# Performance work log

Hardware: AMD Instinct MI355X
Metric: run time of the kernel (lower is better)

The kernel has to match this reference:

```python
import jax, jax.numpy as jnp
import numpy as np
import math

D_MODEL = 512
N_HEADS = 8
FACTOR = 5
B, L_Q, L_K = 8, 4096, 4096


def setup_inputs() -> dict:
    key = jax.random.key(0)
    ks = jax.random.split(key, 9)
    s = 0.02
    sample_k = max(1, int(FACTOR * math.log(L_K + 1)))  # 41
    return {
        "query": jax.random.normal(ks[0], (B, L_Q, D_MODEL), jnp.float32),
        "key_in": jax.random.normal(ks[1], (B, L_K, D_MODEL), jnp.float32),
        "value": jax.random.normal(ks[2], (B, L_K, D_MODEL), jnp.float32),
        "W_Q": jax.random.normal(ks[3], (D_MODEL, D_MODEL), jnp.float32) * s,
        "W_K": jax.random.normal(ks[4], (D_MODEL, D_MODEL), jnp.float32) * s,
        "W_V": jax.random.normal(ks[5], (D_MODEL, D_MODEL), jnp.float32) * s,
        "W_out": jax.random.normal(ks[6], (D_MODEL, D_MODEL), jnp.float32) * s,
        "b_out": jnp.zeros((D_MODEL,), jnp.float32),
        "sample_idx": jax.random.randint(ks[8], (L_Q, sample_k), 0, L_K),
    }


def reference(query, key_in, value, W_Q, W_K, W_V, W_out, b_out, sample_idx):
    b, lq, _ = query.shape
    lk = key_in.shape[1]
    H = N_HEADS
    E = D_MODEL // H
    # projections -> [B, H, L, E]
    Q = (query @ W_Q).reshape(b, lq, H, E).transpose(0, 2, 1, 3)
    K = (key_in @ W_K).reshape(b, lk, H, E).transpose(0, 2, 1, 3)
    V = (value @ W_V).reshape(b, lk, H, E).transpose(0, 2, 1, 3)

    u = max(1, int(FACTOR * math.log(lq + 1)))  # top-u queries (41)

    # sparsity proxy M(q_i, K) on randomly sampled keys
    K_sample = K[:, :, sample_idx, :]                      # [B,H,L_Q,S,E]
    QK_sample = jnp.einsum('bhqe,bhqse->bhqs', Q, K_sample)
    M = QK_sample.max(axis=-1) - QK_sample.mean(axis=-1)   # [B,H,L_Q]
    _, M_top = jax.lax.top_k(M, u)                         # [B,H,u]

    # attention for the top-u queries only
    Q_reduce = jnp.take_along_axis(Q, M_top[..., None], axis=2)  # [B,H,u,E]
    scale = 1.0 / math.sqrt(E)
    scores = jnp.einsum('bhue,bhke->bhuk', Q_reduce, K) * scale
    attn = jax.nn.softmax(scores, axis=-1)  # dropout is identity (eval)
    ctx_top = jnp.einsum('bhuk,bhke->bhue', attn, V)       # [B,H,u,E]

    # mean-value context for the lazy queries, scatter-update the active ones
    ctx = jnp.broadcast_to(V.mean(axis=2, keepdims=True), (b, H, lq, E))
    bi = jnp.arange(b)[:, None, None]
    hi = jnp.arange(H)[None, :, None]
    ctx = ctx.at[bi, hi, M_top].set(ctx_top)

    ctx = ctx.transpose(0, 2, 1, 3).reshape(b, lq, H * E)
    return ctx @ W_out + b_out
```

## Files before the change

kernel.cpp:

```cpp
#include <hip/hip_runtime.h>
#include <cstdint>
#include <cstddef>

#define D_MODEL 512
#define NHEADS  8
#define EDIM    64
#define BATCH   8
#define LSEQ    4096

typedef unsigned short u16;
typedef __attribute__((ext_vector_type(8))) short short8;
typedef __attribute__((ext_vector_type(4))) float f32x4;

__device__ __forceinline__ u16 bf16_rne(float x) {
  unsigned int u = __float_as_uint(x);
  u += 0x7FFFu + ((u >> 16) & 1u);
  return (u16)(u >> 16);
}
__device__ __forceinline__ void split2(float x, u16& h, u16& l) {
  h = bf16_rne(x);
  float hf = __uint_as_float((unsigned int)h << 16);
  l = bf16_rne(x - hf);
}

__global__ __launch_bounds__(256) void cvt_w(
    const float* __restrict__ W0, const float* __restrict__ W1,
    const float* __restrict__ W2, const float* __restrict__ W3,
    u16* __restrict__ out) {
  const float* W = (blockIdx.z == 0) ? W0 : ((blockIdx.z == 1) ? W1 :
                   ((blockIdx.z == 2) ? W2 : W3));
  u16* P = out + (size_t)blockIdx.z * 524288;
  __shared__ float tile[64][65];
  const int k0 = blockIdx.x * 64, n0 = blockIdx.y * 64;
  const int t = threadIdx.x;
  const int tr = t >> 4, tc = (t & 15) * 4;
#pragma unroll
  for (int j = 0; j < 4; ++j) {
    int kr = tr + j * 16;
    float4 v = *(const float4*)(W + (size_t)(k0 + kr) * 512 + n0 + tc);
    tile[kr][tc + 0] = v.x; tile[kr][tc + 1] = v.y;
    tile[kr][tc + 2] = v.z; tile[kr][tc + 3] = v.w;
  }
  __syncthreads();
#pragma unroll
  for (int j = 0; j < 4; ++j) {
    int nr = tr + j * 16;
    ushort4 h, l;
    split2(tile[tc + 0][nr], h.x, l.x);
    split2(tile[tc + 1][nr], h.y, l.y);
    split2(tile[tc + 2][nr], h.z, l.z);
    split2(tile[tc + 3][nr], h.w, l.w);
    size_t off = (size_t)(n0 + nr) * 512 + k0 + tc;
    *(ushort4*)(P + off) = h;
    *(ushort4*)(P + 262144 + off) = l;
  }
}

__device__ __forceinline__ void gld_lds16(const char* g, char* l) {
  __builtin_amdgcn_global_load_lds((const __attribute__((address_space(1))) void*)g,
                                   (__attribute__((address_space(3))) void*)l, 16, 0, 0);
}

__global__ __launch_bounds__(256, 2) void gemm_fused(
    const float* __restrict__ X0, const float* __restrict__ X1,
    const float* __restrict__ X2, const u16* __restrict__ WPbase,
    float* __restrict__ Y0, float* __restrict__ Y1, float* __restrict__ Y2) {
  __shared__ u16 Ah[2][128 * 40];
  __shared__ u16 Al[2][128 * 40];
  __shared__ u16 Bh[2][128 * 32];
  __shared__ u16 Bl[2][128 * 32];
  const int z = blockIdx.z;
  const float* X = (z == 0) ? X0 : ((z == 1) ? X1 : X2);
  float* Y = (z == 0) ? Y0 : ((z == 1) ? Y1 : Y2);
  const u16* WP = WPbase + (size_t)z * 524288;

  const int tid = threadIdx.x;
  const int lane = tid & 63, wv = tid >> 6;
  const int wm = (wv & 1) * 64, wn = (wv >> 1) * 64;
  const int bn = blockIdx.x * 128, bm = blockIdx.y * 128;
  const int fr = lane & 15, quad = lane >> 4;
  const int sRow = tid >> 2, sColB = (tid & 3) * 16;
  const int ar = tid >> 1, ac = (tid & 1) * 16;

  f32x4 acc[16];
#pragma unroll
  for (int i = 0; i < 16; ++i) acc[i] = (f32x4){0.f, 0.f, 0.f, 0.f};

  const u16* Wh = WP;
  const u16* Wl = WP + 262144;
  const float* Arow = X + (size_t)(bm + ar) * 512 + ac;

  union V8 { ushort4 v4[2]; short8 v8; };

  {
    float4 x0 = *(const float4*)(Arow);
    float4 x1 = *(const float4*)(Arow + 4);
    float4 x2 = *(const float4*)(Arow + 8);
    float4 x3 = *(const float4*)(Arow + 12);
#pragma unroll
    for (int j = 0; j < 2; ++j) {
      const size_t rB = (size_t)(bn + j * 64 + sRow) * 512;
      const int lo = (j * 256 + wv * 64) * 16;
      gld_lds16((const char*)(Wh + rB) + sColB, (char*)Bh[0] + lo);
      gld_lds16((const char*)(Wl + rB) + sColB, (char*)Bl[0] + lo);
    }
    V8 h0, l0, h1, l1;
    split2(x0.x, h0.v4[0].x, l0.v4[0].x);
    split2(x0.y, h0.v4[0].y, l0.v4[0].y);
    split2(x0.z, h0.v4[0].z, l0.v4[0].z);
    split2(x0.w, h0.v4[0].w, l0.v4[0].w);
    split2(x1.x, h0.v4[1].x, l0.v4[1].x);
    split2(x1.y, h0.v4[1].y, l0.v4[1].y);
    split2(x1.z, h0.v4[1].z, l0.v4[1].z);
    split2(x1.w, h0.v4[1].w, l0.v4[1].w);
    split2(x2.x, h1.v4[0].x, l1.v4[0].x);
    split2(x2.y, h1.v4[0].y, l1.v4[0].y);
    split2(x2.z, h1.v4[0].z, l1.v4[0].z);
    split2(x2.w, h1.v4[0].w, l1.v4[0].w);
    split2(x3.x, h1.v4[1].x, l1.v4[1].x);
    split2(x3.y, h1.v4[1].y, l1.v4[1].y);
    split2(x3.z, h1.v4[1].z, l1.v4[1].z);
    split2(x3.w, h1.v4[1].w, l1.v4[1].w);
    *(short8*)&Ah[0][ar * 40 + ac]     = h0.v8;
    *(short8*)&Ah[0][ar * 40 + ac + 8] = h1.v8;
    *(short8*)&Al[0][ar * 40 + ac]     = l0.v8;
    *(short8*)&Al[0][ar * 40 + ac + 8] = l1.v8;
  }
  __syncthreads();

  for (int kk = 0; kk < 16; ++kk) {
    const int cur = kk & 1, nxt = cur ^ 1;
    float4 x0, x1, x2, x3;
    if (kk < 15) {
      x0 = *(const float4*)(Arow + (kk + 1) * 32);
      x1 = *(const float4*)(Arow + (kk + 1) * 32 + 4);
      x2 = *(const float4*)(Arow + (kk + 1) * 32 + 8);
      x3 = *(const float4*)(Arow + (kk + 1) * 32 + 12);
#pragma unroll
      for (int j = 0; j < 2; ++j) {
        const size_t rB = (size_t)(bn + j * 64 + sRow) * 512 + (kk + 1) * 32;
        const int lo = (j * 256 + wv * 64) * 16;
        gld_lds16((const char*)(Wh + rB) + sColB, (char*)Bh[nxt] + lo);
        gld_lds16((const char*)(Wl + rB) + sColB, (char*)Bl[nxt] + lo);
      }
    }
    short8 ah[4], al[4], bh4[4], bl4[4];
#pragma unroll
    for (int mi = 0; mi < 4; ++mi) {
      ah[mi] = *(const short8*)&Ah[cur][(wm + mi * 16 + fr) * 40 + quad * 8];
      al[mi] = *(const short8*)&Al[cur][(wm + mi * 16 + fr) * 40 + quad * 8];
    }
#pragma unroll
    for (int ni = 0; ni < 4; ++ni) {
      bh4[ni] = *(const short8*)&Bh[cur][(wn + ni * 16 + fr) * 32 + quad * 8];
      bl4[ni] = *(const short8*)&Bl[cur][(wn + ni * 16 + fr) * 32 + quad * 8];
    }
#pragma unroll
    for (int mi = 0; mi < 4; ++mi)
#pragma unroll
      for (int ni = 0; ni < 4; ++ni)
        acc[mi * 4 + ni] = __builtin_amdgcn_mfma_f32_16x16x32_bf16(
            ah[mi], bh4[ni], acc[mi * 4 + ni], 0, 0, 0);
#pragma unroll
    for (int mi = 0; mi < 4; ++mi)
#pragma unroll
      for (int ni = 0; ni < 4; ++ni)
        acc[mi * 4 + ni] = __builtin_amdgcn_mfma_f32_16x16x32_bf16(
            ah[mi], bl4[ni], acc[mi * 4 + ni], 0, 0, 0);
#pragma unroll
    for (int mi = 0; mi < 4; ++mi)
#pragma unroll
      for (int ni = 0; ni < 4; ++ni)
        acc[mi * 4 + ni] = __builtin_amdgcn_mfma_f32_16x16x32_bf16(
            al[mi], bh4[ni], acc[mi * 4 + ni], 0, 0, 0);
    if (kk < 15) {
      V8 h0, l0, h1, l1;
      split2(x0.x, h0.v4[0].x, l0.v4[0].x);
      split2(x0.y, h0.v4[0].y, l0.v4[0].y);
      split2(x0.z, h0.v4[0].z, l0.v4[0].z);
      split2(x0.w, h0.v4[0].w, l0.v4[0].w);
      split2(x1.x, h0.v4[1].x, l0.v4[1].x);
      split2(x1.y, h0.v4[1].y, l0.v4[1].y);
      split2(x1.z, h0.v4[1].z, l0.v4[1].z);
      split2(x1.w, h0.v4[1].w, l0.v4[1].w);
      split2(x2.x, h1.v4[0].x, l1.v4[0].x);
      split2(x2.y, h1.v4[0].y, l1.v4[0].y);
      split2(x2.z, h1.v4[0].z, l1.v4[0].z);
      split2(x2.w, h1.v4[0].w, l1.v4[0].w);
      split2(x3.x, h1.v4[1].x, l1.v4[1].x);
      split2(x3.y, h1.v4[1].y, l1.v4[1].y);
      split2(x3.z, h1.v4[1].z, l1.v4[1].z);
      split2(x3.w, h1.v4[1].w, l1.v4[1].w);
      *(short8*)&Ah[nxt][ar * 40 + ac]     = h0.v8;
      *(short8*)&Ah[nxt][ar * 40 + ac + 8] = h1.v8;
      *(short8*)&Al[nxt][ar * 40 + ac]     = l0.v8;
      *(short8*)&Al[nxt][ar * 40 + ac + 8] = l1.v8;
    }
    __syncthreads();
  }
#pragma unroll
  for (int mi = 0; mi < 4; ++mi)
#pragma unroll
    for (int ni = 0; ni < 4; ++ni) {
      const f32x4 a = acc[mi * 4 + ni];
      float* yp = Y + (size_t)(bm + wm + mi * 16 + quad * 4) * 512 + (bn + wn + ni * 16 + fr);
#pragma unroll
      for (int r = 0; r < 4; ++r) yp[(size_t)r * 512] = a[r];
    }
}

__global__ __launch_bounds__(256) void qk_sample_half(
    const float* __restrict__ Q, const float* __restrict__ K,
    const int* __restrict__ sidx, float* __restrict__ M, int S, int hg) {
  const int blk = blockIdx.x;
  const int lane = threadIdx.x & 63;
  const int b = blk & 7;
  const int q = ((blk >> 3) << 2) + (threadIdx.x >> 6);
  const int s = lane >> 5;
  const int hl = (lane >> 3) & 3;
  const int d = lane & 7;
  const int h = hg * 4 + hl;
  const int col = hg * 256 + hl * 64 + d * 8;

  const float* Qp = Q + ((size_t)b * LSEQ + q) * D_MODEL + col;
  const float4 q0 = *(const float4*)Qp;
  const float4 q1 = *(const float4*)(Qp + 4);
  const float* Kb = K + (size_t)b * LSEQ * D_MODEL + col;
  const int* sp = sidx + (size_t)q * S;

  auto rowp = [&](int j) -> const float* {
    int jj = j + s;
    int row = sp[(jj < S) ? jj : (S - 1)];
    return Kb + (size_t)row * D_MODEL;
  };

  const float* pr0 = rowp(0);
  float4 a0 = *(const float4*)pr0, b0 = *(const float4*)(pr0 + 4);
  const float* pr1 = rowp(2);
  float4 a1 = *(const float4*)pr1, b1 = *(const float4*)(pr1 + 4);

  float mx = -3.4e38f, sum = 0.0f;
  for (int j = 0; j < S; j += 2) {
    const float4 ca = a0, cb = b0;
    a0 = a1; b0 = b1;
    const float* pn = rowp(j + 4);
    a1 = *(const float4*)pn;
    b1 = *(const float4*)(pn + 4);
    float p = ca.x * q0.x + ca.y * q0.y + ca.z * q0.z + ca.w * q0.w +
              cb.x * q1.x + cb.y * q1.y + cb.z * q1.z + cb.w * q1.w;
    p += __shfl_xor(p, 1, 64);
    p += __shfl_xor(p, 2, 64);
    p += __shfl_xor(p, 4, 64);
    if (j + s < S) {
      mx = fmaxf(mx, p);
      sum += p;
    }
  }
  mx = fmaxf(mx, __shfl_xor(mx, 32, 64));
  sum += __shfl_xor(sum, 32, 64);
  if (s == 0 && d == 0)
    M[((size_t)(b * NHEADS + h)) * LSEQ + q] = mx - sum / (float)S;
}

__global__ __launch_bounds__(256) void topk_kernel(
    const float* __restrict__ M, int* __restrict__ Mtop, int U) {
  __shared__ float vals[LSEQ];
  __shared__ float wbest[4];
  __shared__ int widx[4];
  int bh = blockIdx.x;
  int t = threadIdx.x;
  const int w = t >> 6, lane = t & 63;
  for (int i = t; i < LSEQ; i += 256) vals[i] = M[(size_t)bh * LSEQ + i];
  __syncthreads();
  for (int it = 0; it < U; ++it) {
    float best = -3.4e38f; int bi = 0x7fffffff;
    for (int i = t; i < LSEQ; i += 256) {
      float v = vals[i];
      if (v > best) { best = v; bi = i; }
    }
#pragma unroll
    for (int o = 1; o < 64; o <<= 1) {
      float ov = __shfl_xor(best, o, 64);
      int oi = __shfl_xor(bi, o, 64);
      if (ov > best || (ov == best && oi < bi)) { best = ov; bi = oi; }
    }
    if (lane == 0) { wbest[w] = best; widx[w] = bi; }
    __syncthreads();
    if (t == 0) {
      float B = wbest[0]; int I = widx[0];
#pragma unroll
      for (int w2 = 1; w2 < 4; ++w2)
        if (wbest[w2] > B || (wbest[w2] == B && widx[w2] < I)) {
          B = wbest[w2]; I = widx[w2];
        }
      Mtop[(size_t)bh * U + it] = I;
      vals[I] = -3.4e38f;
    }
    __syncthreads();
  }
}

__global__ __launch_bounds__(256, 2) void attn_flash(
    const float* __restrict__ Q, const float* __restrict__ K,
    const float* __restrict__ V, const int* __restrict__ Mtop,
    float* __restrict__ part_ctx, float* __restrict__ part_m,
    float* __restrict__ part_l, int U, int nsplit, int chunks_per_block) {
  __shared__ u16 KhS[64 * 72];
  __shared__ u16 KlS[64 * 72];
  __shared__ float VsS[64 * 68];
  const int bh = blockIdx.y, split = blockIdx.x;
  const int h = bh & (NHEADS - 1), b = bh >> 3;
  const int t = threadIdx.x, w = t >> 6, lane = t & 63;
  const int fr = lane & 15, quad = lane >> 4;

  const int qi = w * 16 + fr;
  const int qrow = (qi < U) ? Mtop[(size_t)bh * U + qi] : Mtop[(size_t)bh * U];
  const float4* Qr = (const float4*)(Q + ((size_t)(b * LSEQ) + qrow) * D_MODEL + h * EDIM);
  float4 qa = Qr[quad * 2], qb = Qr[quad * 2 + 1];
  float4 qc = Qr[quad * 2 + 8], qd = Qr[quad * 2 + 9];
  short8 qh0, ql0, qh1, ql1;
  {
    u16 hh, ll;
    split2(qa.x, hh, ll); qh0[0] = (short)hh; ql0[0] = (short)ll;
    split2(qa.y, hh, ll); qh0[1] = (short)hh; ql0[1] = (short)ll;
    split2(qa.z, hh, ll); qh0[2] = (short)hh; ql0[2] = (short)ll;
    split2(qa.w, hh, ll); qh0[3] = (short)hh; ql0[3] = (short)ll;
    split2(qb.x, hh, ll); qh0[4] = (short)hh; ql0[4] = (short)ll;
    split2(qb.y, hh, ll); qh0[5] = (short)hh; ql0[5] = (short)ll;
    split2(qb.z, hh, ll); qh0[6] = (short)hh; ql0[6] = (short)ll;
    split2(qb.w, hh, ll); qh0[7] = (short)hh; ql0[7] = (short)ll;
    split2(qc.x, hh, ll); qh1[0] = (short)hh; ql1[0] = (short)ll;
    split2(qc.y, hh, ll); qh1[1] = (short)hh; ql1[1] = (short)ll;
    split2(qc.z, hh, ll); qh1[2] = (short)hh; ql1[2] = (short)ll;
    split2(qc.w, hh, ll); qh1[3] = (short)hh; ql1[3] = (short)ll;
    split2(qd.x, hh, ll); qh1[4] = (short)hh; ql1[4] = (short)ll;
    split2(qd.y, hh, ll); qh1[5] = (short)hh; ql1[5] = (short)ll;
    split2(qd.z, hh, ll); qh1[6] = (short)hh; ql1[6] = (short)ll;
    split2(qd.w, hh, ll); qh1[7] = (short)hh; ql1[7] = (short)ll;
  }

  float4 c4[16];
#pragma unroll
  for (int i = 0; i < 16; ++i) c4[i] = make_float4(0.f, 0.f, 0.f, 0.f);
  float m = -1e30f, l = 0.0f;

  const int r = t >> 2, cg = t & 3;

  const int k_base = split * (chunks_per_block * 64);
  for (int c = 0; c < chunks_per_block; ++c) {
    const int k0 = k_base + c * 64;
    const float4* Kg4 = (const float4*)(K + ((size_t)(b * LSEQ) + k0 + r) * D_MODEL + h * EDIM);
    const float4* Vg4 = (const float4*)(V + ((size_t)(b * LSEQ) + k0 + r) * D_MODEL + h * EDIM);
#pragma unroll
    for (int i = 0; i < 4; ++i) {
      const int f4 = cg + 4 * i;
      float4 kv = Kg4[f4];
      float4 vv = Vg4[f4];
      ushort4 hh, ll;
      split2(kv.x, hh.x, ll.x);
      split2(kv.y, hh.y, ll.y);
      split2(kv.z, hh.z, ll.z);
      split2(kv.w, hh.w, ll.w);
      *(ushort4*)&KhS[r * 72 + f4 * 4] = hh;
      *(ushort4*)&KlS[r * 72 + f4 * 4] = ll;
      *(float4*)&VsS[r * 68 + f4 * 4] = vv;
    }
    __syncthreads();

    f32x4 acc[4];
#pragma unroll
    for (int mt = 0; mt < 4; ++mt) acc[mt] = (f32x4){0.f, 0.f, 0.f, 0.f};
#pragma unroll
    for (int mt = 0; mt < 4; ++mt) {
      short8 kh = *(const short8*)&KhS[(mt * 16 + fr) * 72 + quad * 8];
      short8 kl = *(const short8*)&KlS[(mt * 16 + fr) * 72 + quad * 8];
      acc[mt] = __builtin_amdgcn_mfma_f32_16x16x32_bf16(kh, qh0, acc[mt], 0, 0, 0);
      acc[mt] = __builtin_amdgcn_mfma_f32_16x16x32_bf16(kh, ql0, acc[mt], 0, 0, 0);
      acc[mt] = __builtin_amdgcn_mfma_f32_16x16x32_bf16(kl, qh0, acc[mt], 0, 0, 0);
    }
#pragma unroll
    for (int mt = 0; mt < 4; ++mt) {
      short8 kh = *(const short8*)&KhS[(mt * 16 + fr) * 72 + 32 + quad * 8];
      short8 kl = *(const short8*)&KlS[(mt * 16 + fr) * 72 + 32 + quad * 8];
      acc[mt] = __builtin_amdgcn_mfma_f32_16x16x32_bf16(kh, qh1, acc[mt], 0, 0, 0);
      acc[mt] = __builtin_amdgcn_mfma_f32_16x16x32_bf16(kh, ql1, acc[mt], 0, 0, 0);
      acc[mt] = __builtin_amdgcn_mfma_f32_16x16x32_bf16(kl, qh1, acc[mt], 0, 0, 0);
    }

    float cm = -3.4e38f;
#pragma unroll
    for (int mt = 0; mt < 4; ++mt) {
#pragma unroll
      for (int rr = 0; rr < 4; ++rr) {
        float s = acc[mt][rr] * 0.125f;
        acc[mt][rr] = s;
        cm = fmaxf(cm, s);
      }
    }
    cm = fmaxf(cm, __shfl_xor(cm, 16, 64));
    cm = fmaxf(cm, __shfl_xor(cm, 32, 64));
    float mn = fmaxf(m, cm);
    if (mn > m) {
      float f = __expf(m - mn);
      l *= f;
#pragma unroll
      for (int i = 0; i < 16; ++i) {
        c4[i].x *= f; c4[i].y *= f; c4[i].z *= f; c4[i].w *= f;
      }
      m = mn;
    }
    float psum = 0.0f;
#pragma unroll
    for (int mt = 0; mt < 4; ++mt) {
#pragma unroll
      for (int rr = 0; rr < 4; ++rr) {
        float p = __expf(acc[mt][rr] - m);
        acc[mt][rr] = p;
        psum += p;
      }
    }
    l += psum;

#pragma unroll
    for (int mt = 0; mt < 4; ++mt) {
#pragma unroll
      for (int rr = 0; rr < 4; ++rr) {
        const int krow = mt * 16 + quad * 4 + rr;
        const float4* vr = (const float4*)&VsS[krow * 68];
        const float p = acc[mt][rr];
#pragma unroll
        for (int i = 0; i < 16; ++i) {
          float4 vv = vr[i];
          c4[i].x += p * vv.x; c4[i].y += p * vv.y;
          c4[i].z += p * vv.z; c4[i].w += p * vv.w;
        }
      }
    }
    __syncthreads();
  }

#pragma unroll
  for (int i = 0; i < 16; ++i) {
    c4[i].x += __shfl_xor(c4[i].x, 16, 64);
    c4[i].y += __shfl_xor(c4[i].y, 16, 64);
    c4[i].z += __shfl_xor(c4[i].z, 16, 64);
    c4[i].w += __shfl_xor(c4[i].w, 16, 64);
    c4[i].x += __shfl_xor(c4[i].x, 32, 64);
    c4[i].y += __shfl_xor(c4[i].y, 32, 64);
    c4[i].z += __shfl_xor(c4[i].z, 32, 64);
    c4[i].w += __shfl_xor(c4[i].w, 32, 64);
  }
  l += __shfl_xor(l, 16, 64);
  l += __shfl_xor(l, 32, 64);

  if (quad == 0 && qi < U) {
    part_m[(size_t)(bh * nsplit + split) * 64 + qi] = m;
    part_l[(size_t)(bh * nsplit + split) * 64 + qi] = l;
  }
  float* pc = part_ctx + (size_t)(bh * nsplit + split) * 4096;
  if (quad == 0) {
#pragma unroll
    for (int ii = 0; ii < 16; ++ii) pc[ii * 64 + qi] = (&c4[ii >> 2].x)[ii & 3];
  } else if (quad == 1) {
#pragma unroll
    for (int ii = 0; ii < 16; ++ii) pc[(16 + ii) * 64 + qi] = (&c4[4 + (ii >> 2)].x)[ii & 3];
  } else if (quad == 2) {
#pragma unroll
    for (int ii = 0; ii < 16; ++ii) pc[(32 + ii) * 64 + qi] = (&c4[8 + (ii >> 2)].x)[ii & 3];
  } else {
#pragma unroll
    for (int ii = 0; ii < 16; ++ii) pc[(48 + ii) * 64 + qi] = (&c4[12 + (ii >> 2)].x)[ii & 3];
  }
}

__global__ __launch_bounds__(256) void attn_combine(
    const float* __restrict__ part_ctx, const float* __restrict__ part_m,
    const float* __restrict__ part_l, float* __restrict__ ctxTop,
    int U, int nsplit) {
  __shared__ float F[16][64];
  const int bh = blockIdx.x;
  const int t = threadIdx.x, lane = t & 63, grp = t >> 6;
  if (grp == 0) {
    float M = -3.4e38f;
    for (int s = 0; s < nsplit; ++s)
      M = fmaxf(M, part_m[(size_t)(bh * nsplit + s) * 64 + lane]);
    float L = 0.0f;
    for (int s = 0; s < nsplit; ++s)
      L += part_l[(size_t)(bh * nsplit + s) * 64 + lane] *
           __expf(part_m[(size_t)(bh * nsplit + s) * 64 + lane] - M);
    float invL = 1.0f / L;
    for (int s = 0; s < nsplit; ++s)
      F[s][lane] = __expf(part_m[(size_t)(bh * nsplit + s) * 64 + lane] - M) * invL;
  }
  __syncthreads();
  for (int ei = 0; ei < 16; ++ei) {
    int e = grp * 16 + ei;
    float acc = 0.0f;
    for (int s = 0; s < nsplit; ++s)
      acc += F[s][lane] * part_ctx[(size_t)(bh * nsplit + s) * 4096 + e * 64 + lane];
    if (lane < U) ctxTop[((size_t)bh * U + lane) * 64 + e] = acc;
  }
}

__global__ __launch_bounds__(256) void vmean_part(
    const float* __restrict__ V, float* __restrict__ Vm) {
  __shared__ float part[4][EDIM];
  const int bh = blockIdx.x, chunk = blockIdx.y;
  const int h = bh & (NHEADS - 1), b = bh >> 3;
  const int t = threadIdx.x;
  const int e = t & 63, c = t >> 6;
  float s = 0.0f;
  const int k0 = chunk * 512 + c * 128;
  for (int k = k0; k < k0 + 128; ++k)
    s += V[((size_t)b * LSEQ + k) * D_MODEL + h * EDIM + e];
  part[c][e] = s;
  __syncthreads();
  if (c == 0)
    atomicAdd(&Vm[(size_t)bh * EDIM + e],
              (part[0][e] + part[1][e] + part[2][e] + part[3][e]) *
                  (1.0f / (float)LSEQ));
}

__global__ __launch_bounds__(256) void base_out_kernel(
    const float* __restrict__ Vm, const float* __restrict__ Wout,
    const float* __restrict__ bout, float* __restrict__ base) {
  __shared__ float cb[D_MODEL];
  int b = blockIdx.x;
  int t = threadIdx.x;
  for (int d = t; d < D_MODEL; d += 256) cb[d] = Vm[(size_t)b * D_MODEL + d];
  __syncthreads();
  for (int n = t; n < D_MODEL; n += 256) {
    float s = bout[n];
    for (int d = 0; d < D_MODEL; ++d) s += cb[d] * Wout[(size_t)d * D_MODEL + n];
    base[(size_t)b * D_MODEL + n] = s;
  }
}

__global__ __launch_bounds__(256) void fill_out(
    const float* __restrict__ base, float* __restrict__ out) {
  size_t i = (size_t)blockIdx.x * 256 + threadIdx.x;
  int n4 = (int)(i & 127);
  size_t bq = i >> 7;
  int b = (int)(bq >> 12);
  float4 v = ((const float4*)base)[(size_t)b * 128 + n4];
  ((float4*)out)[i] = v;
}

__global__ __launch_bounds__(256, 1) void delta_out_mfma(
    const float* __restrict__ ctxTop, const float* __restrict__ Vm,
    const int* __restrict__ Mtop, const u16* __restrict__ WoutTP,
    float* __restrict__ out, int U) {
  __shared__ u16 Dh[64 * 72];
  __shared__ u16 Dl[64 * 72];
  __shared__ int qr[64];
  const int bh = blockIdx.x;
  const int h = bh & (NHEADS - 1), b = bh >> 3;
  const int t = threadIdx.x, lane = t & 63, wv = t >> 6;
  const int fr = lane & 15, quad = lane >> 4;

  {
    const int r = t >> 2, c0 = (t & 3) * 16;
#pragma unroll
    for (int j = 0; j < 4; ++j) {
      float4 v = make_float4(0.f, 0.f, 0.f, 0.f);
      if (r < U) {
        float4 cv = *(const float4*)(ctxTop + ((size_t)bh * U + r) * EDIM + c0 + j * 4);
        float4 mv = *(const float4*)(Vm + (size_t)bh * EDIM + c0 + j * 4);
        v = make_float4(cv.x - mv.x, cv.y - mv.y, cv.z - mv.z, cv.w - mv.w);
      }
      ushort4 hh, ll;
      split2(v.x, hh.x, ll.x);
      split2(v.y, hh.y, ll.y);
      split2(v.z, hh.z, ll.z);
      split2(v.w, hh.w, ll.w);
      *(ushort4*)&Dh[r * 72 + c0 + j * 4] = hh;
      *(ushort4*)&Dl[r * 72 + c0 + j * 4] = ll;
    }
  }
  if (t < 64) qr[t] = (t < U) ? Mtop[(size_t)bh * U + t] : -1;
  __syncthreads();

  f32x4 acc[32];
#pragma unroll
  for (int i = 0; i < 32; ++i) acc[i] = (f32x4){0.f, 0.f, 0.f, 0.f};

  const u16* Wh = WoutTP;
  const u16* Wl = WoutTP + 262144;

#pragma unroll
  for (int ks = 0; ks < 2; ++ks) {
    short8 a_h[4], a_l[4];
#pragma unroll
    for (int mt = 0; mt < 4; ++mt) {
      a_h[mt] = *(const short8*)&Dh[(mt * 16 + fr) * 72 + ks * 32 + quad * 8];
      a_l[mt] = *(const short8*)&Dl[(mt * 16 + fr) * 72 + ks * 32 + quad * 8];
    }
#pragma unroll
    for (int nt = 0; nt < 8; ++nt) {
      const int n = wv * 128 + nt * 16 + fr;
      const size_t off = (size_t)n * 512 + h * EDIM + ks * 32 + quad * 8;
      short8 b_h = *(const short8*)&Wh[off];
      short8 b_l = *(const short8*)&Wl[off];
#pragma unroll
      for (int mt = 0; mt < 4; ++mt) {
        acc[mt * 8 + nt] = __builtin_amdgcn_mfma_f32_16x16x32_bf16(
            a_h[mt], b_h, acc[mt * 8 + nt], 0, 0, 0);
        acc[mt * 8 + nt] = __builtin_amdgcn_mfma_f32_16x16x32_bf16(
            a_h[mt], b_l, acc[mt * 8 + nt], 0, 0, 0);
        acc[mt * 8 + nt] = __builtin_amdgcn_mfma_f32_16x16x32_bf16(
            a_l[mt], b_h, acc[mt * 8 + nt], 0, 0, 0);
      }
    }
  }

  int qreg[16];
#pragma unroll
  for (int mt = 0; mt < 4; ++mt)
#pragma unroll
    for (int r4 = 0; r4 < 4; ++r4) qreg[mt * 4 + r4] = qr[mt * 16 + quad * 4 + r4];
#pragma unroll
  for (int mt = 0; mt < 4; ++mt)
#pragma unroll
    for (int nt = 0; nt < 8; ++nt) {
      const f32x4 a = acc[mt * 8 + nt];
      const int n = wv * 128 + nt * 16 + fr;
#pragma unroll
      for (int r4 = 0; r4 < 4; ++r4) {
        const int q = qreg[mt * 4 + r4];
        if (q >= 0)
          atomicAdd(out + ((size_t)b * LSEQ + q) * D_MODEL + n, a[r4]);
      }
    }
}

extern "C" void kernel_launch(void* const* d_in, const int* in_sizes, int n_in,
                              void* d_out, int out_size, void* d_ws, size_t ws_size,
                              hipStream_t stream) {
  const float* query  = (const float*)d_in[0];
  const float* key_in = (const float*)d_in[1];
  const float* value  = (const float*)d_in[2];
  const float* W_Q    = (const float*)d_in[3];
  const float* W_K    = (const float*)d_in[4];
  const float* W_V    = (const float*)d_in[5];
  const float* W_out  = (const float*)d_in[6];
  const float* b_out  = (const float*)d_in[7];
  const int*   sidx   = (const int*)d_in[8];
  float* out = (float*)d_out;

  const int S = in_sizes[8] / LSEQ;
  const int U = S;

  char* ws = (char*)d_ws;
  size_t o = 0;
  float* Qf     = (float*)(ws + o); o += (size_t)BATCH * LSEQ * D_MODEL * 4;
  float* Kf     = (float*)(ws + o); o += (size_t)BATCH * LSEQ * D_MODEL * 4;
  float* Vf     = (float*)(ws + o); o += (size_t)BATCH * LSEQ * D_MODEL * 4;
  int*   Mtop   = (int*)  (ws + o); o += ((size_t)64 * U * 4 + 255) & ~255ULL;
  float* ctxTop = (float*)(ws + o); o += ((size_t)64 * U * EDIM * 4 + 255) & ~255ULL;
  float* Vm     = (float*)(ws + o); o += 16384;
  float* baseO  = (float*)(ws + o); o += 16384;
  u16*   Wpl    = (u16*)  (ws + o); o += (size_t)4 * 524288 * 2;
  size_t unionOff = o;

  float* M = (float*)(ws + unionOff);
  int nsplit = 16;
  for (;;) {
    size_t need = unionOff + 2 * ((size_t)64 * nsplit * 64 * 4)
                  + (size_t)64 * nsplit * 4096 * 4;
    if (need <= ws_size || nsplit == 1) break;
    nsplit >>= 1;
  }
  float* part_m   = (float*)(ws + unionOff);
  float* part_l   = part_m + (size_t)64 * nsplit * 64;
  float* part_ctx = part_l + (size_t)64 * nsplit * 64;
  const int chunks_per_block = 64 / nsplit;

  cvt_w<<<dim3(8, 8, 4), 256, 0, stream>>>(W_Q, W_K, W_V, W_out, Wpl);
  gemm_fused<<<dim3(4, 256, 3), 256, 0, stream>>>(
      query, key_in, value, Wpl, Qf, Kf, Vf);

  qk_sample_half<<<(BATCH * LSEQ) / 4, 256, 0, stream>>>(Qf, Kf, sidx, M, S, 0);
  qk_sample_half<<<(BATCH * LSEQ) / 4, 256, 0, stream>>>(Qf, Kf, sidx, M, S, 1);
  topk_kernel<<<BATCH * NHEADS, 256, 0, stream>>>(M, Mtop, U);
  attn_flash<<<dim3(nsplit, BATCH * NHEADS), 256, 0, stream>>>(
      Qf, Kf, Vf, Mtop, part_ctx, part_m, part_l, U, nsplit, chunks_per_block);
  attn_combine<<<BATCH * NHEADS, 256, 0, stream>>>(
      part_ctx, part_m, part_l, ctxTop, U, nsplit);
  hipMemsetAsync(Vm, 0, (size_t)BATCH * NHEADS * EDIM * 4, stream);
  vmean_part<<<dim3(BATCH * NHEADS, 8), 256, 0, stream>>>(Vf, Vm);
  base_out_kernel<<<BATCH, 256, 0, stream>>>(Vm, W_out, b_out, baseO);
  fill_out<<<(BATCH * LSEQ * (D_MODEL / 4)) / 256, 256, 0, stream>>>(baseO, out);
  delta_out_mfma<<<BATCH * NHEADS, 256, 0, stream>>>(
      ctxTop, Vm, Mtop, Wpl + (size_t)3 * 524288, out, U);
}
```

Baseline: 827.9 us.

## Swizzle packed weight layout for conflict-free LDS reads, drop GEMM double buffering

The weight pre-pack kernel now XOR-swizzles the 8-element k-chunks within each 32-wide group by row, and both the projection GEMM and the output-projection consumer read with the matching swizzled offset. The B tile in LDS (rows of 32 u16) then avoids bank conflicts on the MFMA operand reads. The GEMM also drops its double-buffered LDS pipeline in favour of a single buffer with load, sync, compute, sync per k-step. That halves shared memory and may raise occupancy, but global-load latency is no longer overlapped with MFMA work.

```diff
diff --git a/kernel.cpp b/kernel.cpp
--- a/kernel.cpp
+++ b/kernel.cpp
@@ -50,7 +50,8 @@
     split2(tile[tc + 1][nr], h.y, l.y);
     split2(tile[tc + 2][nr], h.z, l.z);
     split2(tile[tc + 3][nr], h.w, l.w);
-    size_t off = (size_t)(n0 + nr) * 512 + k0 + tc;
+    const int tcs = (tc & 36) | (((((tc >> 3) & 3)) ^ (nr & 3)) << 3);
+    size_t off = (size_t)(n0 + nr) * 512 + k0 + tcs;
     *(ushort4*)(P + off) = h;
     *(ushort4*)(P + 262144 + off) = l;
   }
@@ -65,10 +66,10 @@
     const float* __restrict__ X0, const float* __restrict__ X1,
     const float* __restrict__ X2, const u16* __restrict__ WPbase,
     float* __restrict__ Y0, float* __restrict__ Y1, float* __restrict__ Y2) {
-  __shared__ u16 Ah[2][128 * 40];
-  __shared__ u16 Al[2][128 * 40];
-  __shared__ u16 Bh[2][128 * 32];
-  __shared__ u16 Bl[2][128 * 32];
+  __shared__ u16 Ah[128 * 40];
+  __shared__ u16 Al[128 * 40];
+  __shared__ u16 Bh[128 * 32];
+  __shared__ u16 Bl[128 * 32];
   const int z = blockIdx.z;
   const float* X = (z == 0) ? X0 : ((z == 1) ? X1 : X2);
   float* Y = (z == 0) ? Y0 : ((z == 1) ? Y1 : Y2);
@@ -79,6 +80,7 @@
   const int wm = (wv & 1) * 64, wn = (wv >> 1) * 64;
   const int bn = blockIdx.x * 128, bm = blockIdx.y * 128;
   const int fr = lane & 15, quad = lane >> 4;
+  const int bq = (quad ^ (fr & 3)) * 8;
   const int sRow = tid >> 2, sColB = (tid & 3) * 16;
   const int ar = tid >> 1, ac = (tid & 1) * 16;
 
@@ -92,17 +94,17 @@
 
   union V8 { ushort4 v4[2]; short8 v8; };
 
-  {
-    float4 x0 = *(const float4*)(Arow);
-    float4 x1 = *(const float4*)(Arow + 4);
-    float4 x2 = *(const float4*)(Arow + 8);
-    float4 x3 = *(const float4*)(Arow + 12);
+  for (int kk = 0; kk < 16; ++kk) {
+    float4 x0 = *(const float4*)(Arow + kk * 32);
+    float4 x1 = *(const float4*)(Arow + kk * 32 + 4);
+    float4 x2 = *(const float4*)(Arow + kk * 32 + 8);
+    float4 x3 = *(const float4*)(Arow + kk * 32 + 12);
 #pragma unroll
     for (int j = 0; j < 2; ++j) {
-      const size_t rB = (size_t)(bn + j * 64 + sRow) * 512;
+      const size_t rB = (size_t)(bn + j * 64 + sRow) * 512 + kk * 32;
       const int lo = (j * 256 + wv * 64) * 16;
-      gld_lds16((const char*)(Wh + rB) + sColB, (char*)Bh[0] + lo);
-      gld_lds16((const char*)(Wl + rB) + sColB, (char*)Bl[0] + lo);
+      gld_lds16((const char*)(Wh + rB) + sColB, (char*)Bh + lo);
+      gld_lds16((const char*)(Wl + rB) + sColB, (char*)Bl + lo);
     }
     V8 h0, l0, h1, l1;
     split2(x0.x, h0.v4[0].x, l0.v4[0].x);
@@ -121,39 +123,21 @@
     split2(x3.y, h1.v4[1].y, l1.v4[1].y);
     split2(x3.z, h1.v4[1].z, l1.v4[1].z);
     split2(x3.w, h1.v4[1].w, l1.v4[1].w);
-    *(short8*)&Ah[0][ar * 40 + ac]     = h0.v8;
-    *(short8*)&Ah[0][ar * 40 + ac + 8] = h1.v8;
-    *(short8*)&Al[0][ar * 40 + ac]     = l0.v8;
-    *(short8*)&Al[0][ar * 40 + ac + 8] = l1.v8;
-  }
-  __syncthreads();
-
-  for (int kk = 0; kk < 16; ++kk) {
-    const int cur = kk & 1, nxt = cur ^ 1;
-    float4 x0, x1, x2, x3;
-    if (kk < 15) {
-      x0 = *(const float4*)(Arow + (kk + 1) * 32);
-      x1 = *(const float4*)(Arow + (kk + 1) * 32 + 4);
-      x2 = *(const float4*)(Arow + (kk + 1) * 32 + 8);
-      x3 = *(const float4*)(Arow + (kk + 1) * 32 + 12);
-#pragma unroll
-      for (int j = 0; j < 2; ++j) {
-        const size_t rB = (size_t)(bn + j * 64 + sRow) * 512 + (kk + 1) * 32;
-        const int lo = (j * 256 + wv * 64) * 16;
-        gld_lds16((const char*)(Wh + rB) + sColB, (char*)Bh[nxt] + lo);
-        gld_lds16((const char*)(Wl + rB) + sColB, (char*)Bl[nxt] + lo);
-      }
-    }
+    *(short8*)&Ah[ar * 40 + ac]     = h0.v8;
+    *(short8*)&Ah[ar * 40 + ac + 8] = h1.v8;
+    *(short8*)&Al[ar * 40 + ac]     = l0.v8;
+    *(short8*)&Al[ar * 40 + ac + 8] = l1.v8;
+    __syncthreads();
     short8 ah[4], al[4], bh4[4], bl4[4];
 #pragma unroll
     for (int mi = 0; mi < 4; ++mi) {
-      ah[mi] = *(const short8*)&Ah[cur][(wm + mi * 16 + fr) * 40 + quad * 8];
-      al[mi] = *(const short8*)&Al[cur][(wm + mi * 16 + fr) * 40 + quad * 8];
+      ah[mi] = *(const short8*)&Ah[(wm + mi * 16 + fr) * 40 + quad * 8];
+      al[mi] = *(const short8*)&Al[(wm + mi * 16 + fr) * 40 + quad * 8];
     }
 #pragma unroll
     for (int ni = 0; ni < 4; ++ni) {
-      bh4[ni] = *(const short8*)&Bh[cur][(wn + ni * 16 + fr) * 32 + quad * 8];
-      bl4[ni] = *(const short8*)&Bl[cur][(wn + ni * 16 + fr) * 32 + quad * 8];
+      bh4[ni] = *(const short8*)&Bh[(wn + ni * 16 + fr) * 32 + bq];
+      bl4[ni] = *(const short8*)&Bl[(wn + ni * 16 + fr) * 32 + bq];
     }
 #pragma unroll
     for (int mi = 0; mi < 4; ++mi)
@@ -173,29 +157,6 @@
       for (int ni = 0; ni < 4; ++ni)
         acc[mi * 4 + ni] = __builtin_amdgcn_mfma_f32_16x16x32_bf16(
             al[mi], bh4[ni], acc[mi * 4 + ni], 0, 0, 0);
-    if (kk < 15) {
-      V8 h0, l0, h1, l1;
-      split2(x0.x, h0.v4[0].x, l0.v4[0].x);
-      split2(x0.y, h0.v4[0].y, l0.v4[0].y);
-      split2(x0.z, h0.v4[0].z, l0.v4[0].z);
-      split2(x0.w, h0.v4[0].w, l0.v4[0].w);
-      split2(x1.x, h0.v4[1].x, l0.v4[1].x);
-      split2(x1.y, h0.v4[1].y, l0.v4[1].y);
-      split2(x1.z, h0.v4[1].z, l0.v4[1].z);
-      split2(x1.w, h0.v4[1].w, l0.v4[1].w);
-      split2(x2.x, h1.v4[0].x, l1.v4[0].x);
-      split2(x2.y, h1.v4[0].y, l1.v4[0].y);
-      split2(x2.z, h1.v4[0].z, l1.v4[0].z);
-      split2(x2.w, h1.v4[0].w, l1.v4[0].w);
-      split2(x3.x, h1.v4[1].x, l1.v4[1].x);
-      split2(x3.y, h1.v4[1].y, l1.v4[1].y);
-      split2(x3.z, h1.v4[1].z, l1.v4[1].z);
-      split2(x3.w, h1.v4[1].w, l1.v4[1].w);
-      *(short8*)&Ah[nxt][ar * 40 + ac]     = h0.v8;
-      *(short8*)&Ah[nxt][ar * 40 + ac + 8] = h1.v8;
-      *(short8*)&Al[nxt][ar * 40 + ac]     = l0.v8;
-      *(short8*)&Al[nxt][ar * 40 + ac + 8] = l1.v8;
-    }
     __syncthreads();
   }
 #pragma unroll
@@ -586,6 +547,7 @@
 
   const u16* Wh = WoutTP;
   const u16* Wl = WoutTP + 262144;
+  const int bq = (quad ^ (fr & 3)) * 8;
 
 #pragma unroll
   for (int ks = 0; ks < 2; ++ks) {
@@ -598,7 +560,7 @@
 #pragma unroll
     for (int nt = 0; nt < 8; ++nt) {
       const int n = wv * 128 + nt * 16 + fr;
-      const size_t off = (size_t)n * 512 + h * EDIM + ks * 32 + quad * 8;
+      const size_t off = (size_t)n * 512 + h * EDIM + ks * 32 + bq;
       short8 b_h = *(const short8*)&Wh[off];
       short8 b_l = *(const short8*)&Wl[off];
 #pragma unroll
```

Result: faster. 738.5 us (-10.8%).
